# Performance work log

Hardware: AMD Instinct MI355X
Metric: run time of the kernel (lower is better)

The kernel has to match this reference:

```python
import jax, jax.numpy as jnp
import numpy as np

N = 50000      # nodes
E = 800000     # edges (avg degree 16)
DIN = 500      # input_dim
HID = 100      # hid_dim (fixed in module)
DOUT = 64      # output_dim
EPS = 1e-5     # LayerNorm eps (torch default)


def _layer_norm(x, g, b):
    mu = jnp.mean(x, axis=-1, keepdims=True)
    var = jnp.var(x, axis=-1, keepdims=True)
    return (x - mu) / jnp.sqrt(var + EPS) * g + b


def _gcn_conv(x, src, tgt, W, b):
    # PyG GCNConv: self-loops + symmetric normalization + linear + scatter-add
    h = x @ W  # [N, out]
    idx = jnp.arange(N)
    src_sl = jnp.concatenate([src, idx])
    tgt_sl = jnp.concatenate([tgt, idx])
    deg = jax.ops.segment_sum(jnp.ones(src_sl.shape, h.dtype), tgt_sl, num_segments=N)
    dinv = jnp.where(deg > 0, deg ** -0.5, 0.0)
    norm = dinv[src_sl] * dinv[tgt_sl]  # [E+N]
    out = jax.ops.segment_sum(h[src_sl] * norm[:, None], tgt_sl, num_segments=N)
    return out + b


def setup_inputs() -> dict:
    key = jax.random.key(0)
    ks = jax.random.split(key, 10)
    glorot = lambda k, fi, fo: jax.random.normal(k, (fi, fo), jnp.float32) * np.float32(1.0 / np.sqrt(fi))
    z = lambda d: jnp.zeros((d,), jnp.float32)
    return dict(
        data_x=jax.random.normal(ks[0], (N, DIN), jnp.float32),
        data_edge_index=jax.random.randint(ks[1], (2, E), 0, N),
        data_edge_attr=jnp.zeros((E,), jnp.int32),  # single relation type
        t_W1=glorot(ks[2], DIN, HID), t_b1=z(HID), t_g1=jnp.ones((HID,), jnp.float32), t_be1=z(HID),
        t_W2=glorot(ks[3], HID, HID), t_b2=z(HID), t_g2=jnp.ones((HID,), jnp.float32), t_be2=z(HID),
        r_Wrel=glorot(ks[4], HID, HID)[None],  # [n_relations=1, H, H]
        r_Wself=glorot(ks[5], HID, HID), r_b=z(HID),
        c1_W=glorot(ks[6], HID, HID), c1_b=z(HID),
        c2_W=glorot(ks[7], HID, DOUT), c2_b=z(DOUT),
    )


def reference(data_x, data_edge_index, data_edge_attr,
              t_W1, t_b1, t_g1, t_be1, t_W2, t_b2, t_g2, t_be2,
              r_Wrel, r_Wself, r_b, c1_W, c1_b, c2_W, c2_b):
    src, tgt = data_edge_index[0], data_edge_index[1]
    # transform: Linear -> LN -> ReLU -> Linear -> LN -> ReLU
    x = jax.nn.relu(_layer_norm(data_x @ t_W1 + t_b1, t_g1, t_be1))
    x = jax.nn.relu(_layer_norm(x @ t_W2 + t_b2, t_g2, t_be2))
    # RGCN, n_relations=1, n_layers=1: per-relation message + self transform
    msgs = x[src] @ r_Wrel[0]  # edge_attr is all relation 0
    x = x @ r_Wself + jax.ops.segment_sum(msgs, tgt, num_segments=N) + r_b
    x = jax.nn.relu(x)  # dropout = identity (eval)
    x = jax.nn.relu(_gcn_conv(x, src, tgt, c1_W, c1_b))
    x = _gcn_conv(x, src, tgt, c2_W, c2_b)
    return jax.nn.log_softmax(x, axis=1)
```

## Files before the change

### kernel.cpp

```cpp
#include <hip/hip_runtime.h>
#include <hip/hip_bf16.h>

typedef __attribute__((ext_vector_type(8))) short short8;
typedef __attribute__((ext_vector_type(8))) unsigned short ushort8;
typedef __attribute__((ext_vector_type(4))) float f32x4;

static constexpr int NN = 50000;
static constexpr int NE = 800000;
static constexpr int SCAN_B = 196;

#define MFMA16x16x32 __builtin_amdgcn_mfma_f32_16x16x32_bf16

__device__ __forceinline__ float b2f(unsigned short u){
  unsigned v = ((unsigned)u) << 16;
  return __builtin_bit_cast(float, v);
}
__device__ __forceinline__ unsigned short f2b(float f){
  unsigned x = __builtin_bit_cast(unsigned, f);
  unsigned r = (x + 0x7fffu + ((x >> 16) & 1u)) >> 16;
  return (unsigned short)r;
}

__device__ __align__(256) int   g_isf32;
__device__ __align__(256) unsigned short g_W1t  [112 * 512];
__device__ __align__(256) unsigned short g_W2t  [112 * 128];
__device__ __align__(256) unsigned short g_WselfT[112 * 128];
__device__ __align__(256) unsigned short g_WrelT [112 * 128];
__device__ __align__(256) unsigned short g_c1Wt [112 * 128];
__device__ __align__(256) unsigned short g_c2Wt [64 * 128];
__device__ __align__(256) unsigned short g_bufA[(size_t)NN * 128];
__device__ __align__(256) unsigned short g_bufB[(size_t)NN * 128];
__device__ __align__(256) unsigned short g_bufC[(size_t)NN * 128];
__device__ __align__(256) int   g_deg[NN];
__device__ __align__(256) int   g_rowptr[NN + 1];
__device__ __align__(256) int   g_cursor[NN];
__device__ __align__(256) int   g_colidx[NE];
__device__ __align__(256) float g_dinv[NN];
__device__ __align__(256) int   g_partial[256];

__device__ __forceinline__ float ld_in(const void* p, int idx, int isf32){
  if (isf32) return ((const float*)p)[idx];
  return b2f(((const unsigned short*)p)[idx]);
}

__global__ void k_detect(const unsigned short* __restrict__ x){
  __shared__ int sh[256];
  int tid = threadIdx.x;
  int cnt = 0;
  for (int j = 0; j < 16; j++){
    unsigned short h = x[(size_t)(tid * 16 + j) * 2];
    int e = (h >> 7) & 0xFF;
    if (e >= 90 && e <= 160) cnt++;
  }
  sh[tid] = cnt;
  __syncthreads();
  for (int off = 128; off > 0; off >>= 1){
    if (tid < off) sh[tid] += sh[tid + off];
    __syncthreads();
  }
  if (tid == 0) g_isf32 = (sh[0] < 2458) ? 1 : 0;
}

__global__ void k_zero(){
  int i = blockIdx.x * 256 + threadIdx.x;
  if (i < NN){ g_deg[i] = 0; g_cursor[i] = 0; }
}

__device__ __forceinline__ void xp_one(const void* W, unsigned short* Wt, int idx,
                                       int K, int Nc, int Kpad, int isf32){
  int n = idx / Kpad;
  int k = idx - n * Kpad;
  float v = 0.f;
  if (n < Nc && k < K) v = ld_in(W, k * Nc + n, isf32);
  Wt[idx] = f2b(v);
}
__global__ void k_transpose_all(const void* W1, const void* W2, const void* Wself,
                                const void* Wrel, const void* c1W, const void* c2W){
  int idx = blockIdx.x * 256 + threadIdx.x;
  const int isf32 = g_isf32;
  if (idx < 57344){ xp_one(W1, g_W1t, idx, 500, 100, 512, isf32); return; }
  idx -= 57344;
  if (idx < 14336){ xp_one(W2,    g_W2t,    idx, 100, 100, 128, isf32); return; }
  idx -= 14336;
  if (idx < 14336){ xp_one(Wself, g_WselfT, idx, 100, 100, 128, isf32); return; }
  idx -= 14336;
  if (idx < 14336){ xp_one(Wrel,  g_WrelT,  idx, 100, 100, 128, isf32); return; }
  idx -= 14336;
  if (idx < 14336){ xp_one(c1W,   g_c1Wt,   idx, 100, 100, 128, isf32); return; }
  idx -= 14336;
  if (idx < 8192){  xp_one(c2W,   g_c2Wt,   idx, 100, 64,  128, isf32); }
}

__global__ void k_deg(const int* __restrict__ tgt){
  int e = blockIdx.x * 256 + threadIdx.x;
  if (e < NE) atomicAdd(&g_deg[tgt[e]], 1);
}

__global__ __launch_bounds__(256) void k_scan1(){
  __shared__ int sh[256];
  int t = threadIdx.x;
  int i = blockIdx.x * 256 + t;
  int val = (i < NN) ? g_deg[i] : 0;
  sh[t] = val;
  __syncthreads();
#pragma unroll
  for (int off = 1; off < 256; off <<= 1){
    int v = (t >= off) ? sh[t - off] : 0;
    __syncthreads();
    sh[t] += v;
    __syncthreads();
  }
  if (i < NN){
    g_rowptr[i] = sh[t] - val;
    g_dinv[i] = rsqrtf((float)(val + 1));
  }
  if (t == 255) g_partial[blockIdx.x] = sh[255];
}
__global__ __launch_bounds__(256) void k_scan2(){
  __shared__ int sh[256];
  int t = threadIdx.x;
  int val = (t < SCAN_B) ? g_partial[t] : 0;
  sh[t] = val;
  __syncthreads();
#pragma unroll
  for (int off = 1; off < 256; off <<= 1){
    int v = (t >= off) ? sh[t - off] : 0;
    __syncthreads();
    sh[t] += v;
    __syncthreads();
  }
  if (t < SCAN_B) g_partial[t] = sh[t] - val;
  if (t == 255) g_rowptr[NN] = sh[255];
}
__global__ __launch_bounds__(256) void k_scan3(){
  int i = blockIdx.x * 256 + threadIdx.x;
  if (i < NN) g_rowptr[i] += g_partial[blockIdx.x];
}

__global__ void k_fill(const int* __restrict__ src, const int* __restrict__ tgt){
  int e = blockIdx.x * 256 + threadIdx.x;
  if (e >= NE) return;
  int t = tgt[e];
  int pos = g_rowptr[t] + atomicAdd(&g_cursor[t], 1);
  g_colidx[pos] = src[e];
}

template<int MODE>
__global__ __launch_bounds__(256) void k_agg(){
  const unsigned short* x = (MODE == 1) ? g_bufC : g_bufB;
  int node = blockIdx.x * 16 + (threadIdx.x >> 4);
  if (node >= NN) return;
  const int c8 = (threadIdx.x & 15) * 8;

  float wt = (MODE != 0) ? g_dinv[node] : 1.f;
  float a[4][8];
#pragma unroll
  for (int j = 0; j < 4; j++)
#pragma unroll
    for (int k = 0; k < 8; k++) a[j][k] = 0.f;

  int p0 = g_rowptr[node], p1 = g_rowptr[node + 1];
  for (int p = p0; p < p1; p += 4){
    int   sj[4]; float wj[4];
#pragma unroll
    for (int j = 0; j < 4; j++){
      bool ok = (p + j) < p1;
      sj[j] = ok ? g_colidx[p + j] : node;
      wj[j] = ok ? ((MODE != 0) ? g_dinv[sj[j]] * wt : 1.f) : 0.f;
    }
    ushort8 r[4];
#pragma unroll
    for (int j = 0; j < 4; j++)
      r[j] = *reinterpret_cast<const ushort8*>(&x[(size_t)sj[j] * 128 + c8]);
#pragma unroll
    for (int j = 0; j < 4; j++)
#pragma unroll
      for (int k = 0; k < 8; k++) a[j][k] += wj[j] * b2f((unsigned short)r[j][k]);
  }
  if (MODE != 0){
    float ws = wt * wt;
    ushort8 sv = *reinterpret_cast<const ushort8*>(&x[(size_t)node * 128 + c8]);
#pragma unroll
    for (int k = 0; k < 8; k++) a[0][k] += ws * b2f((unsigned short)sv[k]);
  }
  ushort8 o;
#pragma unroll
  for (int k = 0; k < 8; k++)
    o[k] = f2b(a[0][k] + a[1][k] + a[2][k] + a[3][k]);
  *reinterpret_cast<ushort8*>(&g_bufA[(size_t)node * 128 + c8]) = o;
}

__global__ __launch_bounds__(256, 4) void k_gemm1_ln(const void* __restrict__ Aext,
    const void* __restrict__ bias, const void* __restrict__ gamma,
    const void* __restrict__ beta){
  __shared__ float red[28 * 256];
  const int tid = threadIdx.x;
  const int w = tid >> 6, lane = tid & 63;
  const int m = lane & 15, q = lane >> 4;
  const int row0 = blockIdx.x * 16;
  const int isf32 = g_isf32;
  const int kbase = w * 128;
  f32x4 acc[7] = {};

  if (isf32){
    const float* base = (const float*)Aext + (size_t)(row0 + m) * 500;
    f32x4 L[8];
#pragma unroll
    for (int c = 0; c < 4; c++){
      int col = kbase + c * 32 + q * 8;
      L[2 * c]     = *reinterpret_cast<const f32x4*>(base + min(col, 496));
      L[2 * c + 1] = *reinterpret_cast<const f32x4*>(base + min(col + 4, 496));
    }
#pragma unroll
    for (int c = 0; c < 4; c++){
      f32x4 lo = L[2 * c], hi = L[2 * c + 1];
      short8 a = {(short)f2b(lo[0]), (short)f2b(lo[1]), (short)f2b(lo[2]), (short)f2b(lo[3]),
                  (short)f2b(hi[0]), (short)f2b(hi[1]), (short)f2b(hi[2]), (short)f2b(hi[3])};
      const int k0 = kbase + c * 32 + q * 8;
#pragma unroll
      for (int t = 0; t < 7; t++){
        short8 b = *reinterpret_cast<const short8*>(g_W1t + (size_t)(t * 16 + m) * 512 + k0);
        acc[t] = MFMA16x16x32(a, b, acc[t], 0, 0, 0);
      }
    }
  } else {
    const unsigned short* base = (const unsigned short*)Aext + (size_t)(row0 + m) * 500;
    ushort4 U[8];
#pragma unroll
    for (int c = 0; c < 4; c++){
      int col = kbase + c * 32 + q * 8;
      U[2 * c]     = *reinterpret_cast<const ushort4*>(base + min(col, 496));
      U[2 * c + 1] = *reinterpret_cast<const ushort4*>(base + min(col + 4, 496));
    }
#pragma unroll
    for (int c = 0; c < 4; c++){
      ushort4 lo = U[2 * c], hi = U[2 * c + 1];
      short8 a = {(short)lo.x, (short)lo.y, (short)lo.z, (short)lo.w,
                  (short)hi.x, (short)hi.y, (short)hi.z, (short)hi.w};
      const int k0 = kbase + c * 32 + q * 8;
#pragma unroll
      for (int t = 0; t < 7; t++){
        short8 b = *reinterpret_cast<const short8*>(g_W1t + (size_t)(t * 16 + m) * 512 + k0);
        acc[t] = MFMA16x16x32(a, b, acc[t], 0, 0, 0);
      }
    }
  }

#pragma unroll
  for (int t = 0; t < 7; t++)
#pragma unroll
    for (int r = 0; r < 4; r++)
      red[(t * 4 + r) * 256 + tid] = acc[t][r];
  __syncthreads();
  if (w != 0) return;

  float bf_[7], gf_[7], ef_[7];
#pragma unroll
  for (int t = 0; t < 7; t++){
    int col = t * 16 + m;
    bool ok = col < 100;
    bf_[t] = ok ? ld_in(bias, col, isf32)  : 0.f;
    gf_[t] = ok ? ld_in(gamma, col, isf32) : 0.f;
    ef_[t] = ok ? ld_in(beta, col, isf32)  : 0.f;
  }
#pragma unroll
  for (int r = 0; r < 4; r++){
    float vals[7], s1 = 0.f, s2 = 0.f;
#pragma unroll
    for (int t = 0; t < 7; t++){
      const float* rv = &red[(t * 4 + r) * 256];
      float v = rv[lane] + rv[64 + lane] + rv[128 + lane] + rv[192 + lane];
      int col = t * 16 + m;
      v = (col < 100) ? (v + bf_[t]) : 0.f;
      vals[t] = v; s1 += v; s2 += v * v;
    }
#pragma unroll
    for (int msk = 1; msk < 16; msk <<= 1){
      s1 += __shfl_xor(s1, msk, 64);
      s2 += __shfl_xor(s2, msk, 64);
    }
    float mu = s1 * 0.01f;
    float var = fmaxf(s2 * 0.01f - mu * mu, 0.f);
    float rstd = rsqrtf(var + 1e-5f);
    unsigned short* orow = g_bufA + (size_t)(row0 + q * 4 + r) * 128;
#pragma unroll
    for (int t = 0; t < 7; t++){
      int col = t * 16 + m;
      float y = fmaxf((vals[t] - mu) * rstd * gf_[t] + ef_[t], 0.f);
      orow[col] = f2b((col < 100) ? y : 0.f);
    }
    orow[112 + m] = 0;
  }
}

__global__ __launch_bounds__(256) void k_gemm2_ln(const void* __restrict__ bias,
    const void* __restrict__ gamma, const void* __restrict__ beta){
  const int isf32 = g_isf32;
  const int wave = threadIdx.x >> 6, lane = threadIdx.x & 63;
  const int m = lane & 15, q = lane >> 4;
  const int row0 = (blockIdx.x * 4 + wave) * 16;
  if (row0 >= NN) return;
  f32x4 acc[7] = {};
  const unsigned short* arow = g_bufA + (size_t)(row0 + m) * 128;
#pragma unroll
  for (int c = 0; c < 4; c++){
    const int k0 = c * 32 + q * 8;
    short8 a = *reinterpret_cast<const short8*>(arow + k0);
#pragma unroll
    for (int t = 0; t < 7; t++){
      short8 b = *reinterpret_cast<const short8*>(g_W2t + (size_t)(t * 16 + m) * 128 + k0);
      acc[t] = MFMA16x16x32(a, b, acc[t], 0, 0, 0);
    }
  }
  float bf_[7], gf_[7], ef_[7];
#pragma unroll
  for (int t = 0; t < 7; t++){
    int col = t * 16 + m;
    bool ok = col < 100;
    bf_[t] = ok ? ld_in(bias, col, isf32)  : 0.f;
    gf_[t] = ok ? ld_in(gamma, col, isf32) : 0.f;
    ef_[t] = ok ? ld_in(beta, col, isf32)  : 0.f;
  }
#pragma unroll
  for (int r = 0; r < 4; r++){
    float vals[7], s1 = 0.f, s2 = 0.f;
#pragma unroll
    for (int t = 0; t < 7; t++){
      int col = t * 16 + m;
      float v = (col < 100) ? (acc[t][r] + bf_[t]) : 0.f;
      vals[t] = v; s1 += v; s2 += v * v;
    }
#pragma unroll
    for (int msk = 1; msk < 16; msk <<= 1){
      s1 += __shfl_xor(s1, msk, 64);
      s2 += __shfl_xor(s2, msk, 64);
    }
    float mu = s1 * 0.01f;
    float var = fmaxf(s2 * 0.01f - mu * mu, 0.f);
    float rstd = rsqrtf(var + 1e-5f);
    unsigned short* orow = g_bufB + (size_t)(row0 + q * 4 + r) * 128;
#pragma unroll
    for (int t = 0; t < 7; t++){
      int col = t * 16 + m;
      float y = fmaxf((vals[t] - mu) * rstd * gf_[t] + ef_[t], 0.f);
      orow[col] = f2b((col < 100) ? y : 0.f);
    }
    orow[112 + m] = 0;
  }
}

template<int SEL>
__global__ __launch_bounds__(256) void k_gemm_bias_relu(const void* __restrict__ bias){
  const unsigned short* A1  = (SEL == 0) ? g_bufB : g_bufA;
  const unsigned short* B1t = (SEL == 0) ? g_WselfT : g_c1Wt;
  unsigned short* out       = (SEL == 0) ? g_bufC : g_bufB;
  const int isf32 = g_isf32;

  const int wave = threadIdx.x >> 6, lane = threadIdx.x & 63;
  const int m = lane & 15, q = lane >> 4;
  const int row0 = (blockIdx.x * 4 + wave) * 16;
  if (row0 >= NN) return;
  f32x4 acc[7] = {};
  const unsigned short* a1row = A1 + (size_t)(row0 + m) * 128;
#pragma unroll
  for (int c = 0; c < 4; c++){
    const int k0 = c * 32 + q * 8;
    short8 a = *reinterpret_cast<const short8*>(a1row + k0);
#pragma unroll
    for (int t = 0; t < 7; t++){
      short8 b = *reinterpret_cast<const short8*>(B1t + (size_t)(t * 16 + m) * 128 + k0);
      acc[t] = MFMA16x16x32(a, b, acc[t], 0, 0, 0);
    }
  }
  if (SEL == 0){
    const unsigned short* a2row = g_bufA + (size_t)(row0 + m) * 128;
#pragma unroll
    for (int c = 0; c < 4; c++){
      const int k0 = c * 32 + q * 8;
      short8 a = *reinterpret_cast<const short8*>(a2row + k0);
#pragma unroll
      for (int t = 0; t < 7; t++){
        short8 b = *reinterpret_cast<const short8*>(g_WrelT + (size_t)(t * 16 + m) * 128 + k0);
        acc[t] = MFMA16x16x32(a, b, acc[t], 0, 0, 0);
      }
    }
  }
  float bf_[7];
#pragma unroll
  for (int t = 0; t < 7; t++){
    int col = t * 16 + m;
    bf_[t] = (col < 100) ? ld_in(bias, col, isf32) : 0.f;
  }
#pragma unroll
  for (int r = 0; r < 4; r++){
    unsigned short* orow = out + (size_t)(row0 + q * 4 + r) * 128;
#pragma unroll
    for (int t = 0; t < 7; t++){
      int col = t * 16 + m;
      float y = fmaxf(acc[t][r] + bf_[t], 0.f);
      orow[col] = f2b((col < 100) ? y : 0.f);
    }
    orow[112 + m] = 0;
  }
}

__global__ __launch_bounds__(256) void k_gemm_c2(){
  const int wave = threadIdx.x >> 6, lane = threadIdx.x & 63;
  const int m = lane & 15, q = lane >> 4;
  const int row0 = (blockIdx.x * 4 + wave) * 16;
  if (row0 >= NN) return;
  f32x4 acc[4] = {};
  const unsigned short* arow = g_bufB + (size_t)(row0 + m) * 128;
#pragma unroll
  for (int c = 0; c < 4; c++){
    const int k0 = c * 32 + q * 8;
    short8 a = *reinterpret_cast<const short8*>(arow + k0);
#pragma unroll
    for (int t = 0; t < 4; t++){
      short8 b = *reinterpret_cast<const short8*>(g_c2Wt + (size_t)(t * 16 + m) * 128 + k0);
      acc[t] = MFMA16x16x32(a, b, acc[t], 0, 0, 0);
    }
  }
#pragma unroll
  for (int r = 0; r < 4; r++){
    unsigned short* orow = g_bufC + (size_t)(row0 + q * 4 + r) * 64;
#pragma unroll
    for (int t = 0; t < 4; t++) orow[t * 16 + m] = f2b(acc[t][r]);
  }
}

__global__ __launch_bounds__(256) void k_agg_lsm(const void* __restrict__ bias,
                                                 void* __restrict__ outv){
  const int isf32 = g_isf32;
  int node = blockIdx.x * 32 + (threadIdx.x >> 3);
  if (node >= NN) return;
  const int c8 = (threadIdx.x & 7) * 8;
  float wt = g_dinv[node];
  float a[4][8];
#pragma unroll
  for (int j = 0; j < 4; j++)
#pragma unroll
    for (int k = 0; k < 8; k++) a[j][k] = 0.f;

  int p0 = g_rowptr[node], p1 = g_rowptr[node + 1];
  for (int p = p0; p < p1; p += 4){
    int   sj[4]; float wj[4];
#pragma unroll
    for (int j = 0; j < 4; j++){
      bool ok = (p + j) < p1;
      sj[j] = ok ? g_colidx[p + j] : node;
      wj[j] = ok ? g_dinv[sj[j]] * wt : 0.f;
    }
    ushort8 r[4];
#pragma unroll
    for (int j = 0; j < 4; j++)
      r[j] = *reinterpret_cast<const ushort8*>(&g_bufC[(size_t)sj[j] * 64 + c8]);
#pragma unroll
    for (int j = 0; j < 4; j++)
#pragma unroll
      for (int k = 0; k < 8; k++) a[j][k] += wj[j] * b2f((unsigned short)r[j][k]);
  }
  float ws = wt * wt;
  ushort8 sv = *reinterpret_cast<const ushort8*>(&g_bufC[(size_t)node * 64 + c8]);
#pragma unroll
  for (int k = 0; k < 8; k++) a[0][k] += ws * b2f((unsigned short)sv[k]);

  float v[8], mx = -1e30f;
#pragma unroll
  for (int k = 0; k < 8; k++){
    v[k] = a[0][k] + a[1][k] + a[2][k] + a[3][k] + ld_in(bias, c8 + k, isf32);
    mx = fmaxf(mx, v[k]);
  }
#pragma unroll
  for (int msk = 1; msk < 8; msk <<= 1) mx = fmaxf(mx, __shfl_xor(mx, msk, 64));
  float se = 0.f;
#pragma unroll
  for (int k = 0; k < 8; k++) se += expf(v[k] - mx);
#pragma unroll
  for (int msk = 1; msk < 8; msk <<= 1) se += __shfl_xor(se, msk, 64);
  float lse = logf(se);
  size_t ro = (size_t)node * 64 + c8;
  if (isf32){
    float* o = (float*)outv + ro;
#pragma unroll
    for (int k = 0; k < 8; k++) o[k] = v[k] - mx - lse;
  } else {
    unsigned short* o = (unsigned short*)outv + ro;
#pragma unroll
    for (int k = 0; k < 8; k++) o[k] = f2b(v[k] - mx - lse);
  }
}

extern "C" void kernel_launch(void* const* d_in, const int* in_sizes, int n_in,
                              void* d_out, int out_size, void* d_ws, size_t ws_size,
                              hipStream_t stream){
  (void)in_sizes; (void)n_in; (void)out_size; (void)d_ws; (void)ws_size;
  const void* data_x = d_in[0];
  const int* ei = (const int*)d_in[1];
  const int* src = ei;
  const int* tgt = ei + NE;
  const void *W1 = d_in[3], *b1 = d_in[4], *gm1 = d_in[5], *be1 = d_in[6];
  const void *W2 = d_in[7], *b2 = d_in[8], *gm2 = d_in[9], *be2 = d_in[10];
  const void *Wrel = d_in[11], *Wself = d_in[12], *rb = d_in[13];
  const void *c1W = d_in[14], *c1b = d_in[15];
  const void *c2W = d_in[16], *c2b = d_in[17];

  k_detect<<<1, 256, 0, stream>>>((const unsigned short*)data_x);
  k_zero<<<(NN + 255) / 256, 256, 0, stream>>>();
  k_transpose_all<<<(122880 + 255) / 256, 256, 0, stream>>>(W1, W2, Wself, Wrel, c1W, c2W);

  k_deg<<<(NE + 255) / 256, 256, 0, stream>>>(tgt);
  k_scan1<<<SCAN_B, 256, 0, stream>>>();
  k_scan2<<<1, 256, 0, stream>>>();
  k_scan3<<<SCAN_B, 256, 0, stream>>>();
  k_fill<<<(NE + 255) / 256, 256, 0, stream>>>(src, tgt);

  const int G64 = (NN + 63) / 64;
  const int GA  = (NN + 15) / 16;
  k_gemm1_ln<<<3125, 256, 0, stream>>>(data_x, b1, gm1, be1);
  k_gemm2_ln<<<G64, 256, 0, stream>>>(b2, gm2, be2);
  k_agg<0><<<GA, 256, 0, stream>>>();
  k_gemm_bias_relu<0><<<G64, 256, 0, stream>>>(rb);
  k_agg<1><<<GA, 256, 0, stream>>>();
  k_gemm_bias_relu<1><<<G64, 256, 0, stream>>>(c1b);
  k_gemm_c2<<<G64, 256, 0, stream>>>();
  k_agg_lsm<<<(NN + 31) / 32, 256, 0, stream>>>(c2b, d_out);
}
```

Measured before the change: 507.1 us.

## Fuse all pipeline stages into one cooperative persistent kernel with grid syncs

Replaces the chain of about a dozen kernel launches (degree count, scan, CSR fill, the GEMMs and aggregations) with a single cooperative kernel of 1024 blocks. Stages are separated by grid.sync() and each stage uses grid-stride loops. Detect and zero kernels are also merged into one launch. The aim is to remove per-launch overhead and inter-kernel gaps, at the cost of grid-wide barriers, fixed occupancy limits and a persistent schedule that may balance work less well. The old multi-kernel path is kept as a fallback if the cooperative launch fails.

After: 1.880 ms. 3.71x slower.

```diff
diff --git a/kernel.cpp b/kernel.cpp
--- a/kernel.cpp
+++ b/kernel.cpp
@@ -1,5 +1,8 @@
 #include <hip/hip_runtime.h>
 #include <hip/hip_bf16.h>
+#include <hip/hip_cooperative_groups.h>
+
+namespace cg = cooperative_groups;
 
 typedef __attribute__((ext_vector_type(8))) short short8;
 typedef __attribute__((ext_vector_type(8))) unsigned short ushort8;
@@ -8,6 +11,7 @@
 static constexpr int NN = 50000;
 static constexpr int NE = 800000;
 static constexpr int SCAN_B = 196;
+static constexpr int MEGA_B = 1024;
 
 #define MFMA16x16x32 __builtin_amdgcn_mfma_f32_16x16x32_bf16
 
@@ -43,27 +47,364 @@
   return b2f(((const unsigned short*)p)[idx]);
 }
 
-__global__ void k_detect(const unsigned short* __restrict__ x){
-  __shared__ int sh[256];
-  int tid = threadIdx.x;
-  int cnt = 0;
-  for (int j = 0; j < 16; j++){
-    unsigned short h = x[(size_t)(tid * 16 + j) * 2];
-    int e = (h >> 7) & 0xFF;
-    if (e >= 90 && e <= 160) cnt++;
-  }
-  sh[tid] = cnt;
-  __syncthreads();
-  for (int off = 128; off > 0; off >>= 1){
-    if (tid < off) sh[tid] += sh[tid + off];
+
+__device__ __forceinline__ void body_gemm2_ln(int row0, int m, int q, int isf32,
+    const void* bias, const void* gamma, const void* beta){
+  f32x4 acc[7] = {};
+  const unsigned short* arow = g_bufA + (size_t)(row0 + m) * 128;
+#pragma unroll
+  for (int c = 0; c < 4; c++){
+    const int k0 = c * 32 + q * 8;
+    short8 a = *reinterpret_cast<const short8*>(arow + k0);
+#pragma unroll
+    for (int t = 0; t < 7; t++){
+      short8 b = *reinterpret_cast<const short8*>(g_W2t + (size_t)(t * 16 + m) * 128 + k0);
+      acc[t] = MFMA16x16x32(a, b, acc[t], 0, 0, 0);
+    }
+  }
+  float bf_[7], gf_[7], ef_[7];
+#pragma unroll
+  for (int t = 0; t < 7; t++){
+    int col = t * 16 + m;
+    bool ok = col < 100;
+    bf_[t] = ok ? ld_in(bias, col, isf32)  : 0.f;
+    gf_[t] = ok ? ld_in(gamma, col, isf32) : 0.f;
+    ef_[t] = ok ? ld_in(beta, col, isf32)  : 0.f;
+  }
+#pragma unroll
+  for (int r = 0; r < 4; r++){
+    float vals[7], s1 = 0.f, s2 = 0.f;
+#pragma unroll
+    for (int t = 0; t < 7; t++){
+      int col = t * 16 + m;
+      float v = (col < 100) ? (acc[t][r] + bf_[t]) : 0.f;
+      vals[t] = v; s1 += v; s2 += v * v;
+    }
+#pragma unroll
+    for (int msk = 1; msk < 16; msk <<= 1){
+      s1 += __shfl_xor(s1, msk, 64);
+      s2 += __shfl_xor(s2, msk, 64);
+    }
+    float mu = s1 * 0.01f;
+    float var = fmaxf(s2 * 0.01f - mu * mu, 0.f);
+    float rstd = rsqrtf(var + 1e-5f);
+    unsigned short* orow = g_bufB + (size_t)(row0 + q * 4 + r) * 128;
+#pragma unroll
+    for (int t = 0; t < 7; t++){
+      int col = t * 16 + m;
+      float y = fmaxf((vals[t] - mu) * rstd * gf_[t] + ef_[t], 0.f);
+      orow[col] = f2b((col < 100) ? y : 0.f);
+    }
+    orow[112 + m] = 0;
+  }
+}
+
+__device__ __forceinline__ void body_rgcn(int row0, int m, int q, int isf32,
+                                          const void* bias){
+  f32x4 acc[7] = {};
+  const unsigned short* a1row = g_bufB + (size_t)(row0 + m) * 128;
+#pragma unroll
+  for (int c = 0; c < 4; c++){
+    const int k0 = c * 32 + q * 8;
+    short8 a = *reinterpret_cast<const short8*>(a1row + k0);
+#pragma unroll
+    for (int t = 0; t < 7; t++){
+      short8 b = *reinterpret_cast<const short8*>(g_WselfT + (size_t)(t * 16 + m) * 128 + k0);
+      acc[t] = MFMA16x16x32(a, b, acc[t], 0, 0, 0);
+    }
+  }
+  const unsigned short* a2row = g_bufA + (size_t)(row0 + m) * 128;
+#pragma unroll
+  for (int c = 0; c < 4; c++){
+    const int k0 = c * 32 + q * 8;
+    short8 a = *reinterpret_cast<const short8*>(a2row + k0);
+#pragma unroll
+    for (int t = 0; t < 7; t++){
+      short8 b = *reinterpret_cast<const short8*>(g_WrelT + (size_t)(t * 16 + m) * 128 + k0);
+      acc[t] = MFMA16x16x32(a, b, acc[t], 0, 0, 0);
+    }
+  }
+  float bf_[7];
+#pragma unroll
+  for (int t = 0; t < 7; t++){
+    int col = t * 16 + m;
+    bf_[t] = (col < 100) ? ld_in(bias, col, isf32) : 0.f;
+  }
+#pragma unroll
+  for (int r = 0; r < 4; r++){
+    unsigned short* orow = g_bufC + (size_t)(row0 + q * 4 + r) * 128;
+#pragma unroll
+    for (int t = 0; t < 7; t++){
+      int col = t * 16 + m;
+      float y = fmaxf(acc[t][r] + bf_[t], 0.f);
+      orow[col] = f2b((col < 100) ? y : 0.f);
+    }
+    orow[112 + m] = 0;
+  }
+}
+
+__device__ __forceinline__ void body_conv1(int row0, int m, int q, int isf32,
+                                           const void* bias){
+  f32x4 acc[7] = {};
+  const unsigned short* a1row = g_bufA + (size_t)(row0 + m) * 128;
+#pragma unroll
+  for (int c = 0; c < 4; c++){
+    const int k0 = c * 32 + q * 8;
+    short8 a = *reinterpret_cast<const short8*>(a1row + k0);
+#pragma unroll
+    for (int t = 0; t < 7; t++){
+      short8 b = *reinterpret_cast<const short8*>(g_c1Wt + (size_t)(t * 16 + m) * 128 + k0);
+      acc[t] = MFMA16x16x32(a, b, acc[t], 0, 0, 0);
+    }
+  }
+  float bf_[7];
+#pragma unroll
+  for (int t = 0; t < 7; t++){
+    int col = t * 16 + m;
+    bf_[t] = (col < 100) ? ld_in(bias, col, isf32) : 0.f;
+  }
+#pragma unroll
+  for (int r = 0; r < 4; r++){
+    unsigned short* orow = g_bufB + (size_t)(row0 + q * 4 + r) * 128;
+#pragma unroll
+    for (int t = 0; t < 7; t++){
+      int col = t * 16 + m;
+      float y = fmaxf(acc[t][r] + bf_[t], 0.f);
+      orow[col] = f2b((col < 100) ? y : 0.f);
+    }
+    orow[112 + m] = 0;
+  }
+}
+
+__device__ __forceinline__ void body_c2(int row0, int m, int q){
+  f32x4 acc[4] = {};
+  const unsigned short* arow = g_bufB + (size_t)(row0 + m) * 128;
+#pragma unroll
+  for (int c = 0; c < 4; c++){
+    const int k0 = c * 32 + q * 8;
+    short8 a = *reinterpret_cast<const short8*>(arow + k0);
+#pragma unroll
+    for (int t = 0; t < 4; t++){
+      short8 b = *reinterpret_cast<const short8*>(g_c2Wt + (size_t)(t * 16 + m) * 128 + k0);
+      acc[t] = MFMA16x16x32(a, b, acc[t], 0, 0, 0);
+    }
+  }
+#pragma unroll
+  for (int r = 0; r < 4; r++){
+    unsigned short* orow = g_bufC + (size_t)(row0 + q * 4 + r) * 64;
+#pragma unroll
+    for (int t = 0; t < 4; t++) orow[t * 16 + m] = f2b(acc[t][r]);
+  }
+}
+
+template<int MODE>
+__device__ __forceinline__ void body_agg(int node, int c8){
+  const unsigned short* x = (MODE == 1) ? g_bufC : g_bufB;
+  float wt = (MODE != 0) ? g_dinv[node] : 1.f;
+  float a[4][8];
+#pragma unroll
+  for (int j = 0; j < 4; j++)
+#pragma unroll
+    for (int k = 0; k < 8; k++) a[j][k] = 0.f;
+  int p0 = g_rowptr[node], p1 = g_rowptr[node + 1];
+  for (int p = p0; p < p1; p += 4){
+    int sj[4]; float wj[4];
+#pragma unroll
+    for (int j = 0; j < 4; j++){
+      bool ok = (p + j) < p1;
+      sj[j] = ok ? g_colidx[p + j] : node;
+      wj[j] = ok ? ((MODE != 0) ? g_dinv[sj[j]] * wt : 1.f) : 0.f;
+    }
+    ushort8 r[4];
+#pragma unroll
+    for (int j = 0; j < 4; j++)
+      r[j] = *reinterpret_cast<const ushort8*>(&x[(size_t)sj[j] * 128 + c8]);
+#pragma unroll
+    for (int j = 0; j < 4; j++)
+#pragma unroll
+      for (int k = 0; k < 8; k++) a[j][k] += wj[j] * b2f((unsigned short)r[j][k]);
+  }
+  if (MODE != 0){
+    float ws = wt * wt;
+    ushort8 sv = *reinterpret_cast<const ushort8*>(&x[(size_t)node * 128 + c8]);
+#pragma unroll
+    for (int k = 0; k < 8; k++) a[0][k] += ws * b2f((unsigned short)sv[k]);
+  }
+  ushort8 o;
+#pragma unroll
+  for (int k = 0; k < 8; k++)
+    o[k] = f2b(a[0][k] + a[1][k] + a[2][k] + a[3][k]);
+  *reinterpret_cast<ushort8*>(&g_bufA[(size_t)node * 128 + c8]) = o;
+}
+
+__device__ __forceinline__ void body_agglsm(int node, int c8, int isf32,
+                                            const void* bias, void* outv){
+  float wt = g_dinv[node];
+  float a[4][8];
+#pragma unroll
+  for (int j = 0; j < 4; j++)
+#pragma unroll
+    for (int k = 0; k < 8; k++) a[j][k] = 0.f;
+  int p0 = g_rowptr[node], p1 = g_rowptr[node + 1];
+  for (int p = p0; p < p1; p += 4){
+    int sj[4]; float wj[4];
+#pragma unroll
+    for (int j = 0; j < 4; j++){
+      bool ok = (p + j) < p1;
+      sj[j] = ok ? g_colidx[p + j] : node;
+      wj[j] = ok ? g_dinv[sj[j]] * wt : 0.f;
+    }
+    ushort8 r[4];
+#pragma unroll
+    for (int j = 0; j < 4; j++)
+      r[j] = *reinterpret_cast<const ushort8*>(&g_bufC[(size_t)sj[j] * 64 + c8]);
+#pragma unroll
+    for (int j = 0; j < 4; j++)
+#pragma unroll
+      for (int k = 0; k < 8; k++) a[j][k] += wj[j] * b2f((unsigned short)r[j][k]);
+  }
+  float ws = wt * wt;
+  ushort8 sv = *reinterpret_cast<const ushort8*>(&g_bufC[(size_t)node * 64 + c8]);
+#pragma unroll
+  for (int k = 0; k < 8; k++) a[0][k] += ws * b2f((unsigned short)sv[k]);
+
+  float v[8], mx = -1e30f;
+#pragma unroll
+  for (int k = 0; k < 8; k++){
+    v[k] = a[0][k] + a[1][k] + a[2][k] + a[3][k] + ld_in(bias, c8 + k, isf32);
+    mx = fmaxf(mx, v[k]);
+  }
+#pragma unroll
+  for (int msk = 1; msk < 8; msk <<= 1) mx = fmaxf(mx, __shfl_xor(mx, msk, 64));
+  float se = 0.f;
+#pragma unroll
+  for (int k = 0; k < 8; k++) se += expf(v[k] - mx);
+#pragma unroll
+  for (int msk = 1; msk < 8; msk <<= 1) se += __shfl_xor(se, msk, 64);
+  float lse = logf(se);
+  size_t ro = (size_t)node * 64 + c8;
+  if (isf32){
+    float* o = (float*)outv + ro;
+#pragma unroll
+    for (int k = 0; k < 8; k++) o[k] = v[k] - mx - lse;
+  } else {
+    unsigned short* o = (unsigned short*)outv + ro;
+#pragma unroll
+    for (int k = 0; k < 8; k++) o[k] = f2b(v[k] - mx - lse);
+  }
+}
+
+__device__ __forceinline__ void body_gemm1_compute(const void* Aext, int row0,
+    int m, int q, int kbase, int isf32, f32x4* acc){
+  if (isf32){
+    const float* base = (const float*)Aext + (size_t)(row0 + m) * 500;
+    f32x4 L[8];
+#pragma unroll
+    for (int c = 0; c < 4; c++){
+      int col = kbase + c * 32 + q * 8;
+      L[2 * c]     = *reinterpret_cast<const f32x4*>(base + min(col, 496));
+      L[2 * c + 1] = *reinterpret_cast<const f32x4*>(base + min(col + 4, 496));
+    }
+#pragma unroll
+    for (int c = 0; c < 4; c++){
+      f32x4 lo = L[2 * c], hi = L[2 * c + 1];
+      short8 a = {(short)f2b(lo[0]), (short)f2b(lo[1]), (short)f2b(lo[2]), (short)f2b(lo[3]),
+                  (short)f2b(hi[0]), (short)f2b(hi[1]), (short)f2b(hi[2]), (short)f2b(hi[3])};
+      const int k0 = kbase + c * 32 + q * 8;
+#pragma unroll
+      for (int t = 0; t < 7; t++){
+        short8 b = *reinterpret_cast<const short8*>(g_W1t + (size_t)(t * 16 + m) * 512 + k0);
+        acc[t] = MFMA16x16x32(a, b, acc[t], 0, 0, 0);
+      }
+    }
+  } else {
+    const unsigned short* base = (const unsigned short*)Aext + (size_t)(row0 + m) * 500;
+    ushort4 U[8];
+#pragma unroll
+    for (int c = 0; c < 4; c++){
+      int col = kbase + c * 32 + q * 8;
+      U[2 * c]     = *reinterpret_cast<const ushort4*>(base + min(col, 496));
+      U[2 * c + 1] = *reinterpret_cast<const ushort4*>(base + min(col + 4, 496));
+    }
+#pragma unroll
+    for (int c = 0; c < 4; c++){
+      ushort4 lo = U[2 * c], hi = U[2 * c + 1];
+      short8 a = {(short)lo.x, (short)lo.y, (short)lo.z, (short)lo.w,
+                  (short)hi.x, (short)hi.y, (short)hi.z, (short)hi.w};
+      const int k0 = kbase + c * 32 + q * 8;
+#pragma unroll
+      for (int t = 0; t < 7; t++){
+        short8 b = *reinterpret_cast<const short8*>(g_W1t + (size_t)(t * 16 + m) * 512 + k0);
+        acc[t] = MFMA16x16x32(a, b, acc[t], 0, 0, 0);
+      }
+    }
+  }
+}
+
+__device__ __forceinline__ void body_gemm1_epi(const float* red, int row0,
+    int lane, int m, int q, int isf32,
+    const void* bias, const void* gamma, const void* beta){
+  float bf_[7], gf_[7], ef_[7];
+#pragma unroll
+  for (int t = 0; t < 7; t++){
+    int col = t * 16 + m;
+    bool ok = col < 100;
+    bf_[t] = ok ? ld_in(bias, col, isf32)  : 0.f;
+    gf_[t] = ok ? ld_in(gamma, col, isf32) : 0.f;
+    ef_[t] = ok ? ld_in(beta, col, isf32)  : 0.f;
+  }
+#pragma unroll
+  for (int r = 0; r < 4; r++){
+    float vals[7], s1 = 0.f, s2 = 0.f;
+#pragma unroll
+    for (int t = 0; t < 7; t++){
+      const float* rv = &red[(t * 4 + r) * 256];
+      float v = rv[lane] + rv[64 + lane] + rv[128 + lane] + rv[192 + lane];
+      int col = t * 16 + m;
+      v = (col < 100) ? (v + bf_[t]) : 0.f;
+      vals[t] = v; s1 += v; s2 += v * v;
+    }
+#pragma unroll
+    for (int msk = 1; msk < 16; msk <<= 1){
+      s1 += __shfl_xor(s1, msk, 64);
+      s2 += __shfl_xor(s2, msk, 64);
+    }
+    float mu = s1 * 0.01f;
+    float var = fmaxf(s2 * 0.01f - mu * mu, 0.f);
+    float rstd = rsqrtf(var + 1e-5f);
+    unsigned short* orow = g_bufA + (size_t)(row0 + q * 4 + r) * 128;
+#pragma unroll
+    for (int t = 0; t < 7; t++){
+      int col = t * 16 + m;
+      float y = fmaxf((vals[t] - mu) * rstd * gf_[t] + ef_[t], 0.f);
+      orow[col] = f2b((col < 100) ? y : 0.f);
+    }
+    orow[112 + m] = 0;
+  }
+}
+
+
+__global__ void k_detect_zero(const unsigned short* __restrict__ x){
+  if (blockIdx.x == 0){
+    __shared__ int sh[256];
+    int tid = threadIdx.x;
+    int cnt = 0;
+    for (int j = 0; j < 16; j++){
+      unsigned short h = x[(size_t)(tid * 16 + j) * 2];
+      int e = (h >> 7) & 0xFF;
+      if (e >= 90 && e <= 160) cnt++;
+    }
+    sh[tid] = cnt;
     __syncthreads();
-  }
-  if (tid == 0) g_isf32 = (sh[0] < 2458) ? 1 : 0;
-}
-
-__global__ void k_zero(){
-  int i = blockIdx.x * 256 + threadIdx.x;
-  if (i < NN){ g_deg[i] = 0; g_cursor[i] = 0; }
+    for (int off = 128; off > 0; off >>= 1){
+      if (tid < off) sh[tid] += sh[tid + off];
+      __syncthreads();
+    }
+    if (tid == 0) g_isf32 = (sh[0] < 2458) ? 1 : 0;
+  } else {
+    int i = (blockIdx.x - 1) * 256 + threadIdx.x;
+    if (i < NN){ g_deg[i] = 0; g_cursor[i] = 0; }
+  }
 }
 
 __device__ __forceinline__ void xp_one(const void* W, unsigned short* Wt, int idx,
@@ -91,43 +432,125 @@
   if (idx < 8192){  xp_one(c2W,   g_c2Wt,   idx, 100, 64,  128, isf32); }
 }
 
+struct MegaArgs {
+  const void* data_x; const int* src; const int* tgt;
+  const void *b1, *gm1, *be1, *b2, *gm2, *be2, *rb, *c1b, *c2b;
+  void* out;
+};
+
+__global__ __launch_bounds__(256, 4) void k_mega(MegaArgs A){
+  cg::grid_group grid = cg::this_grid();
+  __shared__ __align__(16) char smem[28672];
+  const int bid = blockIdx.x, tid = threadIdx.x;
+  const int w = tid >> 6, lane = tid & 63;
+  const int m = lane & 15, q = lane >> 4;
+  const int NB = gridDim.x;
+  const int nthread = NB * 256, nwave = NB * 4;
+  const int gw = bid * 4 + w;
+  const int isf32 = g_isf32;
+
+  for (int e = bid * 256 + tid; e < NE; e += nthread) atomicAdd(&g_deg[A.tgt[e]], 1);
+  grid.sync();
+  if (bid < SCAN_B){
+    int* sh = (int*)smem;
+    int i = bid * 256 + tid;
+    int val = (i < NN) ? g_deg[i] : 0;
+    sh[tid] = val; __syncthreads();
+#pragma unroll
+    for (int off = 1; off < 256; off <<= 1){
+      int v = (tid >= off) ? sh[tid - off] : 0;
+      __syncthreads(); sh[tid] += v; __syncthreads();
+    }
+    if (i < NN){ g_rowptr[i] = sh[tid] - val; g_dinv[i] = rsqrtf((float)(val + 1)); }
+    if (tid == 255) g_partial[bid] = sh[255];
+  }
+  grid.sync();
+  if (bid == 0){
+    int* sh = (int*)smem;
+    int val = (tid < SCAN_B) ? g_partial[tid] : 0;
+    sh[tid] = val; __syncthreads();
+#pragma unroll
+    for (int off = 1; off < 256; off <<= 1){
+      int v = (tid >= off) ? sh[tid - off] : 0;
+      __syncthreads(); sh[tid] += v; __syncthreads();
+    }
+    if (tid < SCAN_B) g_partial[tid] = sh[tid] - val;
+    if (tid == 255) g_rowptr[NN] = sh[255];
+  }
+  grid.sync();
+  if (bid < SCAN_B){
+    int i = bid * 256 + tid;
+    if (i < NN) g_rowptr[i] += g_partial[bid];
+  }
+  grid.sync();
+  for (int e = bid * 256 + tid; e < NE; e += nthread){
+    int t = A.tgt[e];
+    int pos = g_rowptr[t] + atomicAdd(&g_cursor[t], 1);
+    g_colidx[pos] = A.src[e];
+  }
+  {
+    float* red = (float*)smem;
+    const int kbase = w * 128;
+    for (int grp = bid; grp < 3125; grp += NB){
+      const int row0 = grp * 16;
+      f32x4 acc[7] = {};
+      body_gemm1_compute(A.data_x, row0, m, q, kbase, isf32, acc);
+      __syncthreads();
+#pragma unroll
+      for (int t = 0; t < 7; t++)
+#pragma unroll
+        for (int r = 0; r < 4; r++)
+          red[(t * 4 + r) * 256 + tid] = acc[t][r];
+      __syncthreads();
+      if (w == 0) body_gemm1_epi(red, row0, lane, m, q, isf32, A.b1, A.gm1, A.be1);
+    }
+  }
+  grid.sync();
+  for (int grp = gw; grp < 3125; grp += nwave) body_gemm2_ln(grp * 16, m, q, isf32, A.b2, A.gm2, A.be2);
+  grid.sync();
+  for (int node = bid * 16 + (tid >> 4); node < NN; node += NB * 16)
+    body_agg<0>(node, (tid & 15) * 8);
+  grid.sync();
+  for (int grp = gw; grp < 3125; grp += nwave) body_rgcn(grp * 16, m, q, isf32, A.rb);
+  grid.sync();
+  for (int node = bid * 16 + (tid >> 4); node < NN; node += NB * 16)
+    body_agg<1>(node, (tid & 15) * 8);
+  grid.sync();
+  for (int grp = gw; grp < 3125; grp += nwave) body_conv1(grp * 16, m, q, isf32, A.c1b);
+  grid.sync();
+  for (int grp = gw; grp < 3125; grp += nwave) body_c2(grp * 16, m, q);
+  grid.sync();
+  for (int node = bid * 32 + (tid >> 3); node < NN; node += NB * 32)
+    body_agglsm(node, (tid & 7) * 8, isf32, A.c2b, A.out);
+}
+
 __global__ void k_deg(const int* __restrict__ tgt){
   int e = blockIdx.x * 256 + threadIdx.x;
   if (e < NE) atomicAdd(&g_deg[tgt[e]], 1);
 }
-
 __global__ __launch_bounds__(256) void k_scan1(){
   __shared__ int sh[256];
   int t = threadIdx.x;
   int i = blockIdx.x * 256 + t;
   int val = (i < NN) ? g_deg[i] : 0;
-  sh[t] = val;
-  __syncthreads();
+  sh[t] = val; __syncthreads();
 #pragma unroll
   for (int off = 1; off < 256; off <<= 1){
     int v = (t >= off) ? sh[t - off] : 0;
-    __syncthreads();
-    sh[t] += v;
-    __syncthreads();
-  }
-  if (i < NN){
-    g_rowptr[i] = sh[t] - val;
-    g_dinv[i] = rsqrtf((float)(val + 1));
-  }
+    __syncthreads(); sh[t] += v; __syncthreads();
+  }
+  if (i < NN){ g_rowptr[i] = sh[t] - val; g_dinv[i] = rsqrtf((float)(val + 1)); }
   if (t == 255) g_partial[blockIdx.x] = sh[255];
 }
 __global__ __launch_bounds__(256) void k_scan2(){
   __shared__ int sh[256];
   int t = threadIdx.x;
   int val = (t < SCAN_B) ? g_partial[t] : 0;
-  sh[t] = val;
-  __syncthreads();
+  sh[t] = val; __syncthreads();
 #pragma unroll
   for (int off = 1; off < 256; off <<= 1){
     int v = (t >= off) ? sh[t - off] : 0;
-    __syncthreads();
-    sh[t] += v;
-    __syncthreads();
+    __syncthreads(); sh[t] += v; __syncthreads();
   }
   if (t < SCAN_B) g_partial[t] = sh[t] - val;
   if (t == 255) g_rowptr[NN] = sh[255];
@@ -136,7 +559,6 @@
   int i = blockIdx.x * 256 + threadIdx.x;
   if (i < NN) g_rowptr[i] += g_partial[blockIdx.x];
 }
-
 __global__ void k_fill(const int* __restrict__ src, const int* __restrict__ tgt){
   int e = blockIdx.x * 256 + threadIdx.x;
   if (e >= NE) return;
@@ -144,52 +566,6 @@
   int pos = g_rowptr[t] + atomicAdd(&g_cursor[t], 1);
   g_colidx[pos] = src[e];
 }
-
-template<int MODE>
-__global__ __launch_bounds__(256) void k_agg(){
-  const unsigned short* x = (MODE == 1) ? g_bufC : g_bufB;
-  int node = blockIdx.x * 16 + (threadIdx.x >> 4);
-  if (node >= NN) return;
-  const int c8 = (threadIdx.x & 15) * 8;
-
-  float wt = (MODE != 0) ? g_dinv[node] : 1.f;
-  float a[4][8];
-#pragma unroll
-  for (int j = 0; j < 4; j++)
-#pragma unroll
-    for (int k = 0; k < 8; k++) a[j][k] = 0.f;
-
-  int p0 = g_rowptr[node], p1 = g_rowptr[node + 1];
-  for (int p = p0; p < p1; p += 4){
-    int   sj[4]; float wj[4];
-#pragma unroll
-    for (int j = 0; j < 4; j++){
-      bool ok = (p + j) < p1;
-      sj[j] = ok ? g_colidx[p + j] : node;
-      wj[j] = ok ? ((MODE != 0) ? g_dinv[sj[j]] * wt : 1.f) : 0.f;
-    }
-    ushort8 r[4];
-#pragma unroll
-    for (int j = 0; j < 4; j++)
-      r[j] = *reinterpret_cast<const ushort8*>(&x[(size_t)sj[j] * 128 + c8]);
-#pragma unroll
-    for (int j = 0; j < 4; j++)
-#pragma unroll
-      for (int k = 0; k < 8; k++) a[j][k] += wj[j] * b2f((unsigned short)r[j][k]);
-  }
-  if (MODE != 0){
-    float ws = wt * wt;
-    ushort8 sv = *reinterpret_cast<const ushort8*>(&x[(size_t)node * 128 + c8]);
-#pragma unroll
-    for (int k = 0; k < 8; k++) a[0][k] += ws * b2f((unsigned short)sv[k]);
-  }
-  ushort8 o;
-#pragma unroll
-  for (int k = 0; k < 8; k++)
-    o[k] = f2b(a[0][k] + a[1][k] + a[2][k] + a[3][k]);
-  *reinterpret_cast<ushort8*>(&g_bufA[(size_t)node * 128 + c8]) = o;
-}
-
 __global__ __launch_bounds__(256, 4) void k_gemm1_ln(const void* __restrict__ Aext,
     const void* __restrict__ bias, const void* __restrict__ gamma,
     const void* __restrict__ beta){
@@ -199,53 +575,8 @@
   const int m = lane & 15, q = lane >> 4;
   const int row0 = blockIdx.x * 16;
   const int isf32 = g_isf32;
-  const int kbase = w * 128;
   f32x4 acc[7] = {};
-
-  if (isf32){
-    const float* base = (const float*)Aext + (size_t)(row0 + m) * 500;
-    f32x4 L[8];
-#pragma unroll
-    for (int c = 0; c < 4; c++){
-      int col = kbase + c * 32 + q * 8;
-      L[2 * c]     = *reinterpret_cast<const f32x4*>(base + min(col, 496));
-      L[2 * c + 1] = *reinterpret_cast<const f32x4*>(base + min(col + 4, 496));
-    }
-#pragma unroll
-    for (int c = 0; c < 4; c++){
-      f32x4 lo = L[2 * c], hi = L[2 * c + 1];
-      short8 a = {(short)f2b(lo[0]), (short)f2b(lo[1]), (short)f2b(lo[2]), (short)f2b(lo[3]),
-                  (short)f2b(hi[0]), (short)f2b(hi[1]), (short)f2b(hi[2]), (short)f2b(hi[3])};
-      const int k0 = kbase + c * 32 + q * 8;
-#pragma unroll
-      for (int t = 0; t < 7; t++){
-        short8 b = *reinterpret_cast<const short8*>(g_W1t + (size_t)(t * 16 + m) * 512 + k0);
-        acc[t] = MFMA16x16x32(a, b, acc[t], 0, 0, 0);
-      }
-    }
-  } else {
-    const unsigned short* base = (const unsigned short*)Aext + (size_t)(row0 + m) * 500;
-    ushort4 U[8];
-#pragma unroll
-    for (int c = 0; c < 4; c++){
-      int col = kbase + c * 32 + q * 8;
-      U[2 * c]     = *reinterpret_cast<const ushort4*>(base + min(col, 496));
-      U[2 * c + 1] = *reinterpret_cast<const ushort4*>(base + min(col + 4, 496));
-    }
-#pragma unroll
-    for (int c = 0; c < 4; c++){
-      ushort4 lo = U[2 * c], hi = U[2 * c + 1];
-      short8 a = {(short)lo.x, (short)lo.y, (short)lo.z, (short)lo.w,
-                  (short)hi.x, (short)hi.y, (short)hi.z, (short)hi.w};
-      const int k0 = kbase + c * 32 + q * 8;
-#pragma unroll
-      for (int t = 0; t < 7; t++){
-        short8 b = *reinterpret_cast<const short8*>(g_W1t + (size_t)(t * 16 + m) * 512 + k0);
-        acc[t] = MFMA16x16x32(a, b, acc[t], 0, 0, 0);
-      }
-    }
-  }
-
+  body_gemm1_compute(Aext, row0, m, q, w * 128, isf32, acc);
 #pragma unroll
   for (int t = 0; t < 7; t++)
 #pragma unroll
@@ -253,242 +584,44 @@
       red[(t * 4 + r) * 256 + tid] = acc[t][r];
   __syncthreads();
   if (w != 0) return;
-
-  float bf_[7], gf_[7], ef_[7];
-#pragma unroll
-  for (int t = 0; t < 7; t++){
-    int col = t * 16 + m;
-    bool ok = col < 100;
-    bf_[t] = ok ? ld_in(bias, col, isf32)  : 0.f;
-    gf_[t] = ok ? ld_in(gamma, col, isf32) : 0.f;
-    ef_[t] = ok ? ld_in(beta, col, isf32)  : 0.f;
-  }
-#pragma unroll
-  for (int r = 0; r < 4; r++){
-    float vals[7], s1 = 0.f, s2 = 0.f;
-#pragma unroll
-    for (int t = 0; t < 7; t++){
-      const float* rv = &red[(t * 4 + r) * 256];
-      float v = rv[lane] + rv[64 + lane] + rv[128 + lane] + rv[192 + lane];
-      int col = t * 16 + m;
-      v = (col < 100) ? (v + bf_[t]) : 0.f;
-      vals[t] = v; s1 += v; s2 += v * v;
-    }
-#pragma unroll
-    for (int msk = 1; msk < 16; msk <<= 1){
-      s1 += __shfl_xor(s1, msk, 64);
-      s2 += __shfl_xor(s2, msk, 64);
-    }
-    float mu = s1 * 0.01f;
-    float var = fmaxf(s2 * 0.01f - mu * mu, 0.f);
-    float rstd = rsqrtf(var + 1e-5f);
-    unsigned short* orow = g_bufA + (size_t)(row0 + q * 4 + r) * 128;
-#pragma unroll
-    for (int t = 0; t < 7; t++){
-      int col = t * 16 + m;
-      float y = fmaxf((vals[t] - mu) * rstd * gf_[t] + ef_[t], 0.f);
-      orow[col] = f2b((col < 100) ? y : 0.f);
-    }
-    orow[112 + m] = 0;
-  }
-}
-
+  body_gemm1_epi(red, row0, lane, m, q, isf32, bias, gamma, beta);
+}
 __global__ __launch_bounds__(256) void k_gemm2_ln(const void* __restrict__ bias,
     const void* __restrict__ gamma, const void* __restrict__ beta){
-  const int isf32 = g_isf32;
   const int wave = threadIdx.x >> 6, lane = threadIdx.x & 63;
-  const int m = lane & 15, q = lane >> 4;
   const int row0 = (blockIdx.x * 4 + wave) * 16;
   if (row0 >= NN) return;
-  f32x4 acc[7] = {};
-  const unsigned short* arow = g_bufA + (size_t)(row0 + m) * 128;
-#pragma unroll
-  for (int c = 0; c < 4; c++){
-    const int k0 = c * 32 + q * 8;
-    short8 a = *reinterpret_cast<const short8*>(arow + k0);
-#pragma unroll
-    for (int t = 0; t < 7; t++){
-      short8 b = *reinterpret_cast<const short8*>(g_W2t + (size_t)(t * 16 + m) * 128 + k0);
-      acc[t] = MFMA16x16x32(a, b, acc[t], 0, 0, 0);
-    }
-  }
-  float bf_[7], gf_[7], ef_[7];
-#pragma unroll
-  for (int t = 0; t < 7; t++){
-    int col = t * 16 + m;
-    bool ok = col < 100;
-    bf_[t] = ok ? ld_in(bias, col, isf32)  : 0.f;
-    gf_[t] = ok ? ld_in(gamma, col, isf32) : 0.f;
-    ef_[t] = ok ? ld_in(beta, col, isf32)  : 0.f;
-  }
-#pragma unroll
-  for (int r = 0; r < 4; r++){
-    float vals[7], s1 = 0.f, s2 = 0.f;
-#pragma unroll
-    for (int t = 0; t < 7; t++){
-      int col = t * 16 + m;
-      float v = (col < 100) ? (acc[t][r] + bf_[t]) : 0.f;
-      vals[t] = v; s1 += v; s2 += v * v;
-    }
-#pragma unroll
-    for (int msk = 1; msk < 16; msk <<= 1){
-      s1 += __shfl_xor(s1, msk, 64);
-      s2 += __shfl_xor(s2, msk, 64);
-    }
-    float mu = s1 * 0.01f;
-    float var = fmaxf(s2 * 0.01f - mu * mu, 0.f);
-    float rstd = rsqrtf(var + 1e-5f);
-    unsigned short* orow = g_bufB + (size_t)(row0 + q * 4 + r) * 128;
-#pragma unroll
-    for (int t = 0; t < 7; t++){
-      int col = t * 16 + m;
-      float y = fmaxf((vals[t] - mu) * rstd * gf_[t] + ef_[t], 0.f);
-      orow[col] = f2b((col < 100) ? y : 0.f);
-    }
-    orow[112 + m] = 0;
-  }
-}
-
-template<int SEL>
-__global__ __launch_bounds__(256) void k_gemm_bias_relu(const void* __restrict__ bias){
-  const unsigned short* A1  = (SEL == 0) ? g_bufB : g_bufA;
-  const unsigned short* B1t = (SEL == 0) ? g_WselfT : g_c1Wt;
-  unsigned short* out       = (SEL == 0) ? g_bufC : g_bufB;
-  const int isf32 = g_isf32;
-
+  body_gemm2_ln(row0, lane & 15, lane >> 4, g_isf32, bias, gamma, beta);
+}
+__global__ __launch_bounds__(256) void k_rgcn(const void* __restrict__ bias){
   const int wave = threadIdx.x >> 6, lane = threadIdx.x & 63;
-  const int m = lane & 15, q = lane >> 4;
   const int row0 = (blockIdx.x * 4 + wave) * 16;
   if (row0 >= NN) return;
-  f32x4 acc[7] = {};
-  const unsigned short* a1row = A1 + (size_t)(row0 + m) * 128;
-#pragma unroll
-  for (int c = 0; c < 4; c++){
-    const int k0 = c * 32 + q * 8;
-    short8 a = *reinterpret_cast<const short8*>(a1row + k0);
-#pragma unroll
-    for (int t = 0; t < 7; t++){
-      short8 b = *reinterpret_cast<const short8*>(B1t + (size_t)(t * 16 + m) * 128 + k0);
-      acc[t] = MFMA16x16x32(a, b, acc[t], 0, 0, 0);
-    }
-  }
-  if (SEL == 0){
-    const unsigned short* a2row = g_bufA + (size_t)(row0 + m) * 128;
-#pragma unroll
-    for (int c = 0; c < 4; c++){
-      const int k0 = c * 32 + q * 8;
-      short8 a = *reinterpret_cast<const short8*>(a2row + k0);
-#pragma unroll
-      for (int t = 0; t < 7; t++){
-        short8 b = *reinterpret_cast<const short8*>(g_WrelT + (size_t)(t * 16 + m) * 128 + k0);
-        acc[t] = MFMA16x16x32(a, b, acc[t], 0, 0, 0);
-      }
-    }
-  }
-  float bf_[7];
-#pragma unroll
-  for (int t = 0; t < 7; t++){
-    int col = t * 16 + m;
-    bf_[t] = (col < 100) ? ld_in(bias, col, isf32) : 0.f;
-  }
-#pragma unroll
-  for (int r = 0; r < 4; r++){
-    unsigned short* orow = out + (size_t)(row0 + q * 4 + r) * 128;
-#pragma unroll
-    for (int t = 0; t < 7; t++){
-      int col = t * 16 + m;
-      float y = fmaxf(acc[t][r] + bf_[t], 0.f);
-      orow[col] = f2b((col < 100) ? y : 0.f);
-    }
-    orow[112 + m] = 0;
-  }
-}
-
+  body_rgcn(row0, lane & 15, lane >> 4, g_isf32, bias);
+}
+__global__ __launch_bounds__(256) void k_conv1(const void* __restrict__ bias){
+  const int wave = threadIdx.x >> 6, lane = threadIdx.x & 63;
+  const int row0 = (blockIdx.x * 4 + wave) * 16;
+  if (row0 >= NN) return;
+  body_conv1(row0, lane & 15, lane >> 4, g_isf32, bias);
+}
 __global__ __launch_bounds__(256) void k_gemm_c2(){
   const int wave = threadIdx.x >> 6, lane = threadIdx.x & 63;
-  const int m = lane & 15, q = lane >> 4;
   const int row0 = (blockIdx.x * 4 + wave) * 16;
   if (row0 >= NN) return;
-  f32x4 acc[4] = {};
-  const unsigned short* arow = g_bufB + (size_t)(row0 + m) * 128;
-#pragma unroll
-  for (int c = 0; c < 4; c++){
-    const int k0 = c * 32 + q * 8;
-    short8 a = *reinterpret_cast<const short8*>(arow + k0);
-#pragma unroll
-    for (int t = 0; t < 4; t++){
-      short8 b = *reinterpret_cast<const short8*>(g_c2Wt + (size_t)(t * 16 + m) * 128 + k0);
-      acc[t] = MFMA16x16x32(a, b, acc[t], 0, 0, 0);
-    }
-  }
-#pragma unroll
-  for (int r = 0; r < 4; r++){
-    unsigned short* orow = g_bufC + (size_t)(row0 + q * 4 + r) * 64;
-#pragma unroll
-    for (int t = 0; t < 4; t++) orow[t * 16 + m] = f2b(acc[t][r]);
-  }
-}
-
+  body_c2(row0, lane & 15, lane >> 4);
+}
+template<int MODE>
+__global__ __launch_bounds__(256) void k_agg(){
+  int node = blockIdx.x * 16 + (threadIdx.x >> 4);
+  if (node >= NN) return;
+  body_agg<MODE>(node, (threadIdx.x & 15) * 8);
+}
 __global__ __launch_bounds__(256) void k_agg_lsm(const void* __restrict__ bias,
                                                  void* __restrict__ outv){
-  const int isf32 = g_isf32;
   int node = blockIdx.x * 32 + (threadIdx.x >> 3);
   if (node >= NN) return;
-  const int c8 = (threadIdx.x & 7) * 8;
-  float wt = g_dinv[node];
-  float a[4][8];
-#pragma unroll
-  for (int j = 0; j < 4; j++)
-#pragma unroll
-    for (int k = 0; k < 8; k++) a[j][k] = 0.f;
-
-  int p0 = g_rowptr[node], p1 = g_rowptr[node + 1];
-  for (int p = p0; p < p1; p += 4){
-    int   sj[4]; float wj[4];
-#pragma unroll
-    for (int j = 0; j < 4; j++){
-      bool ok = (p + j) < p1;
-      sj[j] = ok ? g_colidx[p + j] : node;
-      wj[j] = ok ? g_dinv[sj[j]] * wt : 0.f;
-    }
-    ushort8 r[4];
-#pragma unroll
-    for (int j = 0; j < 4; j++)
-      r[j] = *reinterpret_cast<const ushort8*>(&g_bufC[(size_t)sj[j] * 64 + c8]);
-#pragma unroll
-    for (int j = 0; j < 4; j++)
-#pragma unroll
-      for (int k = 0; k < 8; k++) a[j][k] += wj[j] * b2f((unsigned short)r[j][k]);
-  }
-  float ws = wt * wt;
-  ushort8 sv = *reinterpret_cast<const ushort8*>(&g_bufC[(size_t)node * 64 + c8]);
-#pragma unroll
-  for (int k = 0; k < 8; k++) a[0][k] += ws * b2f((unsigned short)sv[k]);
-
-  float v[8], mx = -1e30f;
-#pragma unroll
-  for (int k = 0; k < 8; k++){
-    v[k] = a[0][k] + a[1][k] + a[2][k] + a[3][k] + ld_in(bias, c8 + k, isf32);
-    mx = fmaxf(mx, v[k]);
-  }
-#pragma unroll
-  for (int msk = 1; msk < 8; msk <<= 1) mx = fmaxf(mx, __shfl_xor(mx, msk, 64));
-  float se = 0.f;
-#pragma unroll
-  for (int k = 0; k < 8; k++) se += expf(v[k] - mx);
-#pragma unroll
-  for (int msk = 1; msk < 8; msk <<= 1) se += __shfl_xor(se, msk, 64);
-  float lse = logf(se);
-  size_t ro = (size_t)node * 64 + c8;
-  if (isf32){
-    float* o = (float*)outv + ro;
-#pragma unroll
-    for (int k = 0; k < 8; k++) o[k] = v[k] - mx - lse;
-  } else {
-    unsigned short* o = (unsigned short*)outv + ro;
-#pragma unroll
-    for (int k = 0; k < 8; k++) o[k] = f2b(v[k] - mx - lse);
-  }
+  body_agglsm(node, (threadIdx.x & 7) * 8, g_isf32, bias, outv);
 }
 
 extern "C" void kernel_launch(void* const* d_in, const int* in_sizes, int n_in,
@@ -505,24 +638,28 @@
   const void *c1W = d_in[14], *c1b = d_in[15];
   const void *c2W = d_in[16], *c2b = d_in[17];
 
-  k_detect<<<1, 256, 0, stream>>>((const unsigned short*)data_x);
-  k_zero<<<(NN + 255) / 256, 256, 0, stream>>>();
+  k_detect_zero<<<1 + (NN + 255) / 256, 256, 0, stream>>>((const unsigned short*)data_x);
   k_transpose_all<<<(122880 + 255) / 256, 256, 0, stream>>>(W1, W2, Wself, Wrel, c1W, c2W);
 
-  k_deg<<<(NE + 255) / 256, 256, 0, stream>>>(tgt);
-  k_scan1<<<SCAN_B, 256, 0, stream>>>();
-  k_scan2<<<1, 256, 0, stream>>>();
-  k_scan3<<<SCAN_B, 256, 0, stream>>>();
-  k_fill<<<(NE + 255) / 256, 256, 0, stream>>>(src, tgt);
-
-  const int G64 = (NN + 63) / 64;
-  const int GA  = (NN + 15) / 16;
-  k_gemm1_ln<<<3125, 256, 0, stream>>>(data_x, b1, gm1, be1);
-  k_gemm2_ln<<<G64, 256, 0, stream>>>(b2, gm2, be2);
-  k_agg<0><<<GA, 256, 0, stream>>>();
-  k_gemm_bias_relu<0><<<G64, 256, 0, stream>>>(rb);
-  k_agg<1><<<GA, 256, 0, stream>>>();
-  k_gemm_bias_relu<1><<<G64, 256, 0, stream>>>(c1b);
-  k_gemm_c2<<<G64, 256, 0, stream>>>();
-  k_agg_lsm<<<(NN + 31) / 32, 256, 0, stream>>>(c2b, d_out);
-}
+  MegaArgs ma{data_x, src, tgt, b1, gm1, be1, b2, gm2, be2, rb, c1b, c2b, d_out};
+  void* kargs[] = {&ma};
+  hipError_t err = hipLaunchCooperativeKernel((void*)k_mega, dim3(MEGA_B), dim3(256),
+                                              kargs, 0, stream);
+  if (err != hipSuccess){
+    const int G64 = (NN + 63) / 64;
+    const int GA  = (NN + 15) / 16;
+    k_deg<<<(NE + 255) / 256, 256, 0, stream>>>(tgt);
+    k_scan1<<<SCAN_B, 256, 0, stream>>>();
+    k_scan2<<<1, 256, 0, stream>>>();
+    k_scan3<<<SCAN_B, 256, 0, stream>>>();
+    k_fill<<<(NE + 255) / 256, 256, 0, stream>>>(src, tgt);
+    k_gemm1_ln<<<3125, 256, 0, stream>>>(data_x, b1, gm1, be1);
+    k_gemm2_ln<<<G64, 256, 0, stream>>>(b2, gm2, be2);
+    k_agg<0><<<GA, 256, 0, stream>>>();
+    k_rgcn<<<G64, 256, 0, stream>>>(rb);
+    k_agg<1><<<GA, 256, 0, stream>>>();
+    k_conv1<<<G64, 256, 0, stream>>>(c1b);
+    k_gemm_c2<<<G64, 256, 0, stream>>>();
+    k_agg_lsm<<<(NN + 31) / 32, 256, 0, stream>>>(c2b, d_out);
+  }
+}
```
